# Performance work log

Measured on AMD Instinct MI355X. Metric: run time of the kernel, lower is better.

## Reference

```python
import jax, jax.numpy as jnp
import numpy as np

B, SEQ, NNODES = 4, 12, 1024
SEG_LEN, SEG_NUM = 3, 4
HID, FF, DK, NH, NLAYERS = 64, 2048, 32, 8, 2


def setup_inputs() -> dict:
    key = jax.random.key(0)
    ks = iter(jax.random.split(key, 64))
    def nrm(shape, scale=0.05):
        return jax.random.normal(next(ks), shape, dtype=jnp.float32) * scale
    ones = lambda s: jnp.ones(s, jnp.float32)
    zeros = lambda s: jnp.zeros(s, jnp.float32)
    S, L = 2, NLAYERS
    return {
        'traffic': nrm((B, SEQ, NNODES), 1.0),
        'user': nrm((B, SEQ, NNODES), 1.0),
        'patch_w': nrm((S, HID, SEG_LEN)), 'patch_b': nrm((S, HID)),
        'mha_w': nrm((S, L, 3 * HID, HID)), 'mha_b': nrm((S, L, 3 * HID)),
        'out_w': nrm((S, L, HID, HID)), 'out_b': nrm((S, L, HID)),
        'ff1_w': nrm((S, L, FF, HID)), 'ff1_b': nrm((S, L, FF)),
        'ff2_w': nrm((S, L, HID, FF)), 'ff2_b': nrm((S, L, HID)),
        'ln1_g': ones((S, L, HID)), 'ln1_b': zeros((S, L, HID)),
        'ln2_g': ones((S, L, HID)), 'ln2_b': zeros((S, L, HID)),
        'ga_wq': nrm((S, L, DK, HID)), 'ga_wk': nrm((S, L, DK, HID)), 'ga_wv': nrm((S, L, HID, HID)),
        'ga_ff1_w': nrm((S, L, FF, HID)), 'ga_ff1_b': nrm((S, L, FF)),
        'ga_ff2_w': nrm((S, L, HID, FF)), 'ga_ff2_b': nrm((S, L, HID)),
        'ga_ln1_g': ones((S, L, HID)), 'ga_ln1_b': zeros((S, L, HID)),
        'ga_ln2_g': ones((S, L, HID)), 'ga_ln2_b': zeros((S, L, HID)),
        'ca_wq': nrm((DK, 2 * HID)), 'ca_wk': nrm((DK, 2 * HID)), 'ca_wv': nrm((HID, 2 * HID)),
    }


def _ln(x, g, b, eps=1e-5):
    m = x.mean(-1, keepdims=True)
    v = jnp.mean((x - m) ** 2, -1, keepdims=True)
    return (x - m) / jnp.sqrt(v + eps) * g + b


def _pe(s, d):
    pos = jnp.arange(s, dtype=jnp.float32)[:, None]
    div = jnp.exp(jnp.arange(0, d, 2, dtype=jnp.float32) * (-np.log(10000.0) / d))
    pe = jnp.zeros((s, d), jnp.float32)
    pe = pe.at[:, 0::2].set(jnp.sin(pos * div))
    pe = pe.at[:, 1::2].set(jnp.cos(pos * div))
    return pe


def _mha(x, w, b, wo, bo):
    # standard nn.MultiheadAttention self-attn, batch_first; x: [B,S,H]
    qkv = x @ w.T + b
    q, k, v = jnp.split(qkv, 3, axis=-1)
    def heads(t):
        b_, s_, h_ = t.shape
        return t.reshape(b_, s_, NH, h_ // NH).transpose(0, 2, 1, 3)
    q, k, v = heads(q), heads(k), heads(v)
    scale = 1.0 / jnp.sqrt(jnp.float32(HID // NH))
    att = jax.nn.softmax(jnp.einsum('bhqd,bhkd->bhqk', q, k) * scale, axis=-1)
    o = jnp.einsum('bhqk,bhkd->bhqd', att, v).transpose(0, 2, 1, 3).reshape(x.shape)
    return o @ wo.T + bo


def _enc_layer(x, p):
    # TransformerEncoderLayer_cross, post-norm, dropout=0 (eval)
    x = _ln(x + _mha(x, p['mw'], p['mb'], p['ow'], p['ob']), p['g1'], p['b1'])
    f = jax.nn.relu(x @ p['f1w'].T + p['f1b']) @ p['f2w'].T + p['f2b']
    return _ln(x + f, p['g2'], p['b2'])


def _graph_att(x, p):
    # GraphAttention.forward (bias=None, mask=None, dropout=0)
    q = x @ p['wq'].T
    k = x @ p['wk'].T
    v = x @ p['wv'].T
    dist = jax.nn.softmax(jnp.einsum('bnd,bmd->bnm', q, k) / jnp.sqrt(jnp.float32(DK)), axis=-1)
    att = jnp.einsum('bnm,bmd->bnd', dist, v)
    att = _ln(att, p['g1'], p['b1']) + x
    f = jax.nn.relu(att @ p['f1w'].T + p['f1b']) @ p['f2w'].T + p['f2b']
    return _ln(att + f, p['g2'], p['b2'])


def reference(traffic, user, patch_w, patch_b, mha_w, mha_b, out_w, out_b,
              ff1_w, ff1_b, ff2_w, ff2_b, ln1_g, ln1_b, ln2_g, ln2_b,
              ga_wq, ga_wk, ga_wv, ga_ff1_w, ga_ff1_b, ga_ff2_w, ga_ff2_b,
              ga_ln1_g, ga_ln1_b, ga_ln2_g, ga_ln2_b, ca_wq, ca_wk, ca_wv):
    pe = _pe(SEG_NUM, HID)

    def encode(x, s):
        b, _, d = x.shape
        # DSW_embedding: b (seg_num seg_len) d -> b d seg_num seg_len, then Linear
        seg = x.reshape(b, SEG_NUM, SEG_LEN, d).transpose(0, 3, 1, 2)
        z = seg @ patch_w[s].T + patch_b[s]          # [b, d, seg_num, HID]
        z = z + pe                                    # positional encoding over patches
        for i in range(NLAYERS):
            # temporal attention over the patch axis
            zt = z.reshape(b * d, SEG_NUM, HID)
            zt = _enc_layer(zt, dict(mw=mha_w[s, i], mb=mha_b[s, i], ow=out_w[s, i], ob=out_b[s, i],
                                     f1w=ff1_w[s, i], f1b=ff1_b[s, i], f2w=ff2_w[s, i], f2b=ff2_b[s, i],
                                     g1=ln1_g[s, i], b1=ln1_b[s, i], g2=ln2_g[s, i], b2=ln2_b[s, i]))
            z = zt.reshape(b, d, SEG_NUM, HID)
            # spatial graph attention over the node axis
            zs = z.transpose(0, 2, 1, 3).reshape(b * SEG_NUM, d, HID)
            zs = _graph_att(zs, dict(wq=ga_wq[s, i], wk=ga_wk[s, i], wv=ga_wv[s, i],
                                     f1w=ga_ff1_w[s, i], f1b=ga_ff1_b[s, i], f2w=ga_ff2_w[s, i], f2b=ga_ff2_b[s, i],
                                     g1=ga_ln1_g[s, i], b1=ga_ln1_b[s, i], g2=ga_ln2_g[s, i], b2=ga_ln2_b[s, i]))
            z = zs.reshape(b, SEG_NUM, d, HID).transpose(0, 2, 1, 3)
        return z.mean(axis=2)                         # pool patches -> [b, d, HID]

    enc = jnp.concatenate([encode(traffic, 0), encode(user, 1)], axis=-1)  # [b, d, 2*HID]
    # encoder_attn: SelfAttention(2*HID -> dim_k=32, dim_v=HID)
    q = enc @ ca_wq.T
    k = enc @ ca_wk.T
    v = enc @ ca_wv.T
    dist = jax.nn.softmax(jnp.einsum('bnd,bmd->bnm', q, k) / jnp.sqrt(jnp.float32(DK)), axis=-1)
    return jnp.einsum('bnm,bmd->bnd', dist, v)        # [b, n_nodes, HID]
```

## Files before the change

kernel.cpp:

```cpp
#include <hip/hip_runtime.h>
#include <hip/hip_bf16.h>
#include <math.h>

#define BB 4
#define SEQL 12
#define NN 1024
#define SEGL 3
#define SEGN 4
#define HID 64
#define FFD 2048
#define DKK 32
#define NHH 8
#define HDD 8
#define ZS 1048576

using bf16 = __hip_bfloat16;
__device__ __forceinline__ float b2f(bf16 v) { return __bfloat162float(v); }

typedef __attribute__((ext_vector_type(8))) short s8v;
typedef __attribute__((ext_vector_type(4))) float f4v;
typedef __attribute__((ext_vector_type(4))) unsigned short u4v;

__device__ __forceinline__ unsigned short f2b(float f) {
  bf16 h = __float2bfloat16(f);
  unsigned short u; __builtin_memcpy(&u, &h, 2); return u;
}
__device__ __forceinline__ float us2f(unsigned short u) {
  unsigned int e = ((unsigned int)u) << 16;
  float f; __builtin_memcpy(&f, &e, 4); return f;
}

template <int F>
__device__ __forceinline__ float ldw(const void* p, long i) {
  if (F) return ((const float*)p)[i];
  return b2f(((const bf16*)p)[i]);
}
template <int F>
__device__ __forceinline__ s8v ldfrag(const void* p, long elemOff) {
  if (F) {
    const float* fp = (const float*)p + elemOff;
    f4v u = *(const f4v*)fp, v = *(const f4v*)(fp + 4);
    s8v t;
    t[0]=f2b(u[0]); t[1]=f2b(u[1]); t[2]=f2b(u[2]); t[3]=f2b(u[3]);
    t[4]=f2b(v[0]); t[5]=f2b(v[1]); t[6]=f2b(v[2]); t[7]=f2b(v[3]);
    return t;
  }
  return *(const s8v*)((const unsigned short*)p + elemOff);
}
template <int F>
__device__ __forceinline__ f4v ldb4(const void* p, long i) {
  if (F) return *(const f4v*)((const float*)p + i);
  u4v u = *(const u4v*)((const unsigned short*)p + i);
  f4v r; r[0]=us2f(u[0]); r[1]=us2f(u[1]); r[2]=us2f(u[2]); r[3]=us2f(u[3]);
  return r;
}

__global__ void k_zero(unsigned short* __restrict__ o, int n) {
  int i = blockIdx.x * 256 + threadIdx.x;
  if (i < n) o[i] = 0;
}

__global__ void k_detect(const void* __restrict__ x0, int* __restrict__ flag) {
  int t = threadIdx.x;
  int bad = 0;
  const bf16* p = (const bf16*)x0;
  for (int i = t; i < 512; i += 256) {
    float a = fabsf(b2f(p[i]));
    if (!(a < 1e4f) || (a != 0.f && a < 1e-4f)) bad = 1;
  }
  __shared__ int tot;
  if (t == 0) tot = 0;
  __syncthreads();
  unsigned long long m = __ballot(bad);
  if ((t & 63) == 0) atomicAdd(&tot, __popcll(m));
  __syncthreads();
  if (t == 0) *flag = (tot > 64) ? 1 : 0;
}

template <int F>
__device__ __forceinline__ void wconv_body(const void* __restrict__ w1,
    const void* __restrict__ w2, const void* __restrict__ w3,
    const void* __restrict__ w4, unsigned short* __restrict__ out) {
  int i = blockIdx.x * 256 + threadIdx.x;
  long e8 = (long)i * 8;
  int slot = (int)(e8 >> 17);
  int si = slot >> 2, which = slot & 3;
  long r = e8 & 131071;
  const void* src = (which == 0) ? w1 : (which == 1) ? w2 : (which == 2) ? w3 : w4;
  *(s8v*)(out + e8) = ldfrag<F>(src, (long)si*FFD*HID + r);
}
__global__ __launch_bounds__(256) void k_wconv(const void* w1, const void* w2,
    const void* w3, const void* w4, unsigned short* out,
    const int* __restrict__ flag) {
  if (*flag) wconv_body<1>(w1, w2, w3, w4, out);
  else       wconv_body<0>(w1, w2, w3, w4, out);
}

#define TT 64
#define FRW 64
#define HCS 74

__device__ __forceinline__ void ff_ld(const unsigned short* __restrict__ wc1,
    const unsigned short* __restrict__ wc2, int hb, int srow, int le,
    s8v* r1, s8v* r2) {
  r1[0] = *(const s8v*)(wc1 + (long)(hb + srow)*HID + le*8);
  r1[1] = *(const s8v*)(wc1 + (long)(hb + srow + 8)*HID + le*8);
  r2[0] = *(const s8v*)(wc2 + (long)srow*FFD + hb + le*8);
  r2[1] = *(const s8v*)(wc2 + (long)(srow + 8)*FFD + hb + le*8);
}
__device__ __forceinline__ void ff_wr(char* ldsbuf, int pb, int srow, int swb,
    const s8v* r1, const s8v* r2) {
  char* w1b = ldsbuf + pb*8192;
  char* w2b = ldsbuf + 16384 + pb*8192;
  *(s8v*)(w1b + srow*128 + swb) = r1[0];
  *(s8v*)(w1b + (srow + 8)*128 + swb) = r1[1];
  *(s8v*)(w2b + srow*128 + swb) = r2[0];
  *(s8v*)(w2b + (srow + 8)*128 + swb) = r2[1];
}
template <int F>
__device__ __forceinline__ void ff_compute(const char* ldsbuf, int pb, int hb,
    int col, int quad, int sw, const s8v* bx, unsigned short* hcw,
    const void* __restrict__ B1, long ob1, f4v* acc) {
  const char* w1b = ldsbuf + pb*8192;
  const char* w2b = ldsbuf + 16384 + pb*8192;
#pragma unroll
  for (int t = 0; t < 4; ++t) {
    int row = t*16 + col;
    s8v a10 = *(const s8v*)(w1b + row*128 + ((quad*16) ^ sw));
    s8v a11 = *(const s8v*)(w1b + row*128 + ((64 + quad*16) ^ sw));
    f4v bv = ldb4<F>(B1, ob1 + hb + t*16 + quad*4);
    f4v sv = __builtin_amdgcn_mfma_f32_16x16x32_bf16(a10, bx[0],
               (f4v){0.f,0.f,0.f,0.f}, 0, 0, 0);
    sv = __builtin_amdgcn_mfma_f32_16x16x32_bf16(a11, bx[1], sv, 0, 0, 0);
    unsigned short pk[4];
#pragma unroll
    for (int r = 0; r < 4; ++r) pk[r] = f2b(fmaxf(sv[r] + bv[r], 0.f));
    *(unsigned long long*)&hcw[col*HCS + t*16 + quad*4] =
      (unsigned long long)pk[0] | ((unsigned long long)pk[1] << 16) |
      ((unsigned long long)pk[2] << 32) | ((unsigned long long)pk[3] << 48);
  }
#pragma unroll
  for (int ks2 = 0; ks2 < 2; ++ks2) {
    s8v bh = *(const s8v*)&hcw[col*HCS + ks2*32 + quad*8];
#pragma unroll
    for (int m = 0; m < 4; ++m) {
      int r2 = m*16 + col;
      s8v a2 = *(const s8v*)(w2b + r2*128 + ((ks2*64 + quad*16) ^ sw));
      acc[m] = __builtin_amdgcn_mfma_f32_16x16x32_bf16(a2, bh, acc[m], 0, 0, 0);
    }
  }
}
template <int F>
__device__ __forceinline__ void ff_run(char* ldsbuf,
    const unsigned short* __restrict__ wc1, const unsigned short* __restrict__ wc2,
    const void* __restrict__ B1, long ob1, const s8v* bx, unsigned short* hcw,
    int col, int quad, int sw, int srow, int le, int swb, f4v* acc) {
  s8v c1[2], c2[2], rA1[2], rA2[2], rB1[2], rB2[2];
  ff_ld(wc1, wc2, 0, srow, le, c1, c2);
  ff_wr(ldsbuf, 0, srow, swb, c1, c2);
  ff_ld(wc1, wc2, 64, srow, le, rA1, rA2);
  ff_ld(wc1, wc2, 128, srow, le, rB1, rB2);
  __syncthreads();
  for (int c = 0; c < 32; c += 2) {
    ff_compute<F>(ldsbuf, 0, c*64, col, quad, sw, bx, hcw, B1, ob1, acc);
    ff_wr(ldsbuf, 1, srow, swb, rA1, rA2);
    if (c + 3 < 32) ff_ld(wc1, wc2, (c+3)*64, srow, le, rA1, rA2);
    __syncthreads();
    ff_compute<F>(ldsbuf, 1, (c+1)*64, col, quad, sw, bx, hcw, B1, ob1, acc);
    if (c + 2 < 32) ff_wr(ldsbuf, 0, srow, swb, rB1, rB2);
    if (c + 4 < 32) ff_ld(wc1, wc2, (c+4)*64, srow, le, rB1, rB2);
    __syncthreads();
  }
}

template <int F>
__device__ __forceinline__ void tff_body(float* __restrict__ zb,
    const void* __restrict__ xt, const void* __restrict__ xu,
    const void* __restrict__ pw, const void* __restrict__ pbp,
    const void* __restrict__ W, const void* __restrict__ bq,
    const void* __restrict__ WO, const void* __restrict__ bo,
    const void* __restrict__ g1, const void* __restrict__ b1,
    const unsigned short* __restrict__ wcw, int li,
    const void* __restrict__ B1, const void* __restrict__ B2,
    const void* __restrict__ G, const void* __restrict__ Bt,
    const void* __restrict__ pgf1b, const void* __restrict__ pgf2b,
    const void* __restrict__ pgl2g, const void* __restrict__ pgl2b,
    const void* __restrict__ gwq, const void* __restrict__ gwk,
    const void* __restrict__ gwv,
    unsigned short* __restrict__ qo, unsigned short* __restrict__ ko,
    unsigned short* __restrict__ vto,
    char* lds) {
  int s = blockIdx.x >> 8, blk = blockIdx.x & 255;
  long si = s*2 + li;
  float* z = zb + (long)s*ZS;
  long oW = si*3*HID*HID, obq = si*3*HID, oWO = si*HID*HID, obo = si*HID;
  long og1 = si*HID, ob1 = si*HID;
  const unsigned short* wc1 = wcw + (si*4 + 0)*131072;
  const unsigned short* wc2 = wcw + (si*4 + 1)*131072;
  long fob1 = si*FFD, fob2 = si*HID, fog = si*HID, fobt = si*HID;
  unsigned short (*qkvs)[200] = (unsigned short(*)[200])lds;
  unsigned short (*ao)[72]    = (unsigned short(*)[72])(lds + 25600);
  float (*yb)[68]             = (float(*)[68])(lds + 34816);
  int tid = threadIdx.x;
  int w = tid >> 6, lane = tid & 63;
  int col = lane & 15, quad = lane >> 4;
  long r0 = (long)blk * TT;
  float* stash = (float*)(lds + 59648);
  float* stashW = stash + w*16*68;
  unsigned short* hcw = (unsigned short*)(lds + 32768 + w*2368);
  float* red = (float*)(lds + 42240 + w*4352);
  int lr = lane >> 3, le = lane & 7;
  int srow = w*16 + lr;
  int swb = ((le ^ lr) << 4);
  const int sw = (col & 7) << 4;

  if (li == 0) {
    const void* x = s ? xu : xt;
    long opw = (long)s*HID*SEGL, opb = (long)s*HID;
    float dv = expf((float)(2*(lane >> 1)) * (-logf(10000.f) / (float)HID));
    float pe[4];
#pragma unroll
    for (int g = 0; g < 4; ++g) {
      float ang = (float)g * dv;
      pe[g] = (lane & 1) ? cosf(ang) : sinf(ang);
    }
    float pbv = ldw<F>(pbp, opb + lane);
    float pwv[3];
#pragma unroll
    for (int l = 0; l < 3; ++l) pwv[l] = ldw<F>(pw, opw + lane*3 + l);
#pragma unroll
    for (int rr = 0; rr < 16; ++rr) {
      long tok = r0 + w*16 + rr;
      int b_ = (int)(tok >> 12);
      int n_ = (int)((tok >> 2) & 1023);
      int g_ = (int)(tok & 3);
      float a = pbv;
#pragma unroll
      for (int l = 0; l < 3; ++l)
        a += ldw<F>(x, (long)(b_*SEQL + g_*SEGL + l)*NN + n_) * pwv[l];
      stashW[rr*68 + lane] = a + pe[g_];
    }
    __syncthreads();
  } else {
    long sip = s*2;
    const unsigned short* pw1 = wcw + (sip*4 + 2)*131072;
    const unsigned short* pw2 = wcw + (sip*4 + 3)*131072;
    long pob1 = sip*FFD, pob2 = sip*HID, pog = sip*HID, pobt = sip*HID;
    s8v bxp[2];
    {
      const float* xr = z + (r0 + w*16 + col) * HID;
#pragma unroll
      for (int ks = 0; ks < 2; ++ks) {
        const float* p = xr + ks*32 + quad*8;
        f4v u = *(const f4v*)p, v = *(const f4v*)(p + 4);
        s8v t;
        t[0]=f2b(u[0]); t[1]=f2b(u[1]); t[2]=f2b(u[2]); t[3]=f2b(u[3]);
        t[4]=f2b(v[0]); t[5]=f2b(v[1]); t[6]=f2b(v[2]); t[7]=f2b(v[3]);
        bxp[ks] = t;
      }
    }
    f4v accp[4];
#pragma unroll
    for (int m = 0; m < 4; ++m) accp[m] = (f4v){0.f,0.f,0.f,0.f};
    ff_run<F>(lds, pw1, pw2, pgf1b, pob1, bxp, hcw, col, quad, sw, srow, le, swb, accp);
#pragma unroll
    for (int m = 0; m < 4; ++m)
      *(f4v*)&red[col*68 + m*16 + quad*4] = accp[m];
    float pgg = ldw<F>(pgl2g, pog + lane), pbb = ldw<F>(pgl2b, pobt + lane);
    float pb2 = ldw<F>(pgf2b, pob2 + lane);
#pragma unroll
    for (int rr = 0; rr < 16; ++rr) {
      long grow = r0 + w*16 + rr;
      float val = red[rr*68 + lane] + pb2 + z[grow*HID + lane];
      float sm = val;
#pragma unroll
      for (int off = 32; off; off >>= 1) sm += __shfl_xor(sm, off);
      float m = sm * (1.f/HID);
      float d = val - m;
      float sq = d*d;
#pragma unroll
      for (int off = 32; off; off >>= 1) sq += __shfl_xor(sq, off);
      float rv = rsqrtf(sq*(1.f/HID) + 1e-5f);
      stashW[rr*68 + lane] = d*rv*pgg + pbb;
    }
    __syncthreads();
  }

  s8v bx[4][2];
#pragma unroll
  for (int mt = 0; mt < 4; ++mt) {
    const float* xr = &stash[(mt*16 + col)*68];
#pragma unroll
    for (int ks = 0; ks < 2; ++ks) {
      const float* p = xr + ks*32 + quad*8;
      f4v u = *(const f4v*)p, v = *(const f4v*)(p + 4);
      s8v t;
      t[0]=f2b(u[0]); t[1]=f2b(u[1]); t[2]=f2b(u[2]); t[3]=f2b(u[3]);
      t[4]=f2b(v[0]); t[5]=f2b(v[1]); t[6]=f2b(v[2]); t[7]=f2b(v[3]);
      bx[mt][ks] = t;
    }
  }
#pragma unroll
  for (int nt = 0; nt < 3; ++nt) {
    int cbase = (w*3 + nt) * 16;
    s8v aw[2];
#pragma unroll
    for (int ks = 0; ks < 2; ++ks)
      aw[ks] = ldfrag<F>(W, oW + (long)(cbase + col)*HID + ks*32 + quad*8);
    f4v bv = ldb4<F>(bq, obq + cbase + quad*4);
#pragma unroll
    for (int mt = 0; mt < 4; ++mt) {
      f4v sv = (f4v){0.f,0.f,0.f,0.f};
#pragma unroll
      for (int ks = 0; ks < 2; ++ks)
        sv = __builtin_amdgcn_mfma_f32_16x16x32_bf16(aw[ks], bx[mt][ks], sv, 0, 0, 0);
      unsigned short pk[4];
#pragma unroll
      for (int r = 0; r < 4; ++r) pk[r] = f2b(sv[r] + bv[r]);
      *(unsigned long long*)&qkvs[mt*16 + col][cbase + quad*4] =
        (unsigned long long)pk[0] | ((unsigned long long)pk[1] << 16) |
        ((unsigned long long)pk[2] << 32) | ((unsigned long long)pk[3] << 48);
    }
  }
  __syncthreads();
  if (tid < 128) {
    int gi = tid >> 3, hd = tid & 7;
    int tl = gi * 4;
    float qv[4][8], kv[4][8], vv[4][8];
#pragma unroll
    for (int t4 = 0; t4 < 4; ++t4) {
      s8v qq = *(const s8v*)&qkvs[tl + t4][hd*8];
      s8v kk = *(const s8v*)&qkvs[tl + t4][64 + hd*8];
      s8v vq = *(const s8v*)&qkvs[tl + t4][128 + hd*8];
#pragma unroll
      for (int e = 0; e < 8; ++e) {
        qv[t4][e] = us2f((unsigned short)qq[e]);
        kv[t4][e] = us2f((unsigned short)kk[e]);
        vv[t4][e] = us2f((unsigned short)vq[e]);
      }
    }
    const float sc8 = 0.3535533905932738f;
#pragma unroll
    for (int qt = 0; qt < 4; ++qt) {
      float sc[4]; float mx = -1e30f;
#pragma unroll
      for (int kt = 0; kt < 4; ++kt) {
        float d = 0;
#pragma unroll
        for (int e = 0; e < 8; ++e) d += qv[qt][e]*kv[kt][e];
        sc[kt] = d*sc8; mx = fmaxf(mx, sc[kt]);
      }
      float se = 0;
#pragma unroll
      for (int kt = 0; kt < 4; ++kt) { sc[kt] = expf(sc[kt]-mx); se += sc[kt]; }
      float inv = 1.f/se;
      s8v outp;
#pragma unroll
      for (int e = 0; e < 8; ++e) {
        float o = 0;
#pragma unroll
        for (int kt = 0; kt < 4; ++kt) o += sc[kt]*vv[kt][e];
        outp[e] = (short)f2b(o*inv);
      }
      *(s8v*)&ao[tl + qt][hd*8] = outp;
    }
  }
  __syncthreads();
  s8v awo[2];
#pragma unroll
  for (int ks = 0; ks < 2; ++ks)
    awo[ks] = ldfrag<F>(WO, oWO + (long)(w*16 + col)*HID + ks*32 + quad*8);
  f4v bov = ldb4<F>(bo, obo + w*16 + quad*4);
#pragma unroll
  for (int mt = 0; mt < 4; ++mt) {
    f4v ov = (f4v){0.f,0.f,0.f,0.f};
#pragma unroll
    for (int ks = 0; ks < 2; ++ks) {
      s8v bao = *(const s8v*)&ao[mt*16 + col][ks*32 + quad*8];
      ov = __builtin_amdgcn_mfma_f32_16x16x32_bf16(awo[ks], bao, ov, 0, 0, 0);
    }
    f4v yv;
#pragma unroll
    for (int r = 0; r < 4; ++r) yv[r] = ov[r] + bov[r];
    *(f4v*)&yb[mt*16 + col][w*16 + quad*4] = yv;
  }
  __syncthreads();
  {
    float gg = ldw<F>(g1, og1 + lane), bb2 = ldw<F>(b1, ob1 + lane);
#pragma unroll
    for (int rr = 0; rr < 16; ++rr) {
      int row = w*16 + rr;
      float val = yb[row][lane] + stashW[rr*68 + lane];
      float sm = val;
#pragma unroll
      for (int off = 32; off; off >>= 1) sm += __shfl_xor(sm, off);
      float m = sm*(1.f/HID);
      float d = val - m, sq = d*d;
#pragma unroll
      for (int off = 32; off; off >>= 1) sq += __shfl_xor(sq, off);
      float rv = rsqrtf(sq*(1.f/HID) + 1e-5f);
      stashW[rr*68 + lane] = d*rv*gg + bb2;
    }
  }
  __syncthreads();

  s8v bx2[2];
#pragma unroll
  for (int ks = 0; ks < 2; ++ks) {
    const float* p = &stashW[col*68 + ks*32 + quad*8];
    f4v u = *(const f4v*)p, v = *(const f4v*)(p + 4);
    s8v t;
    t[0]=f2b(u[0]); t[1]=f2b(u[1]); t[2]=f2b(u[2]); t[3]=f2b(u[3]);
    t[4]=f2b(v[0]); t[5]=f2b(v[1]); t[6]=f2b(v[2]); t[7]=f2b(v[3]);
    bx2[ks] = t;
  }

  f4v acc[4];
#pragma unroll
  for (int m = 0; m < 4; ++m) acc[m] = (f4v){0.f,0.f,0.f,0.f};
  ff_run<F>(lds, wc1, wc2, B1, fob1, bx2, hcw, col, quad, sw, srow, le, swb, acc);

#pragma unroll
  for (int m = 0; m < 4; ++m)
    *(f4v*)&red[col*68 + m*16 + quad*4] = acc[m];
  float* finb = (float*)lds;
  {
    float fgg = ldw<F>(G, fog + lane), fbbt = ldw<F>(Bt, fobt + lane);
    float b2v = ldw<F>(B2, fob2 + lane);
#pragma unroll
    for (int rr = 0; rr < 16; ++rr) {
      long grow = r0 + w*16 + rr;
      float val = red[rr*68 + lane] + b2v + stashW[rr*68 + lane];
      float sm = val;
#pragma unroll
      for (int off = 32; off; off >>= 1) sm += __shfl_xor(sm, off);
      float m = sm * (1.f/HID);
      float d = val - m;
      float sq = d*d;
#pragma unroll
      for (int off = 32; off; off >>= 1) sq += __shfl_xor(sq, off);
      float rv = rsqrtf(sq*(1.f/HID) + 1e-5f);
      float fin = d*rv*fgg + fbbt;
      z[grow*HID + lane] = fin;
      finb[(w*16 + rr)*68 + lane] = fin;
    }
  }
  __syncthreads();

  long oq = si*DKK*HID, okk = si*DKK*HID, ovv = si*HID*HID;
  s8v bx3[4][2];
#pragma unroll
  for (int rt = 0; rt < 4; ++rt)
#pragma unroll
    for (int ks = 0; ks < 2; ++ks) {
      const float* p = &finb[(rt*16 + col)*68 + ks*32 + quad*8];
      f4v u = *(const f4v*)p, v = *(const f4v*)(p + 4);
      s8v t;
      t[0]=f2b(u[0]); t[1]=f2b(u[1]); t[2]=f2b(u[2]); t[3]=f2b(u[3]);
      t[4]=f2b(v[0]); t[5]=f2b(v[1]); t[6]=f2b(v[2]); t[7]=f2b(v[3]);
      bx3[rt][ks] = t;
    }
#pragma unroll
  for (int tt = 0; tt < 2; ++tt) {
    int ct = w*2 + tt;
    const void* wp; long wo; int co; int kind;
    if (ct < 2)      { wp = gwq; wo = oq;  co = ct*16;      kind = 0; }
    else if (ct < 4) { wp = gwk; wo = okk; co = (ct-2)*16;  kind = 1; }
    else             { wp = gwv; wo = ovv; co = (ct-4)*16;  kind = 2; }
    s8v aw[2];
#pragma unroll
    for (int ks = 0; ks < 2; ++ks)
      aw[ks] = ldfrag<F>(wp, wo + (long)(co + col)*HID + ks*32 + quad*8);
#pragma unroll
    for (int rt = 0; rt < 4; ++rt) {
      f4v sv = (f4v){0.f,0.f,0.f,0.f};
#pragma unroll
      for (int ks = 0; ks < 2; ++ks)
        sv = __builtin_amdgcn_mfma_f32_16x16x32_bf16(aw[ks], bx3[rt][ks], sv, 0, 0, 0);
      long tok2 = r0 + rt*16 + col;
      int b_ = (int)(tok2 >> 12);
      int n_ = (int)((tok2 >> 2) & 1023);
      int g_ = (int)(tok2 & 3);
      int sgl = s*16 + b_*4 + g_;
      if (kind == 2) {
        long vbase = (long)sgl*HID*NN;
#pragma unroll
        for (int r = 0; r < 4; ++r)
          vto[vbase + (long)(co + quad*4 + r)*NN + n_] = f2b(sv[r]);
      } else {
        long row = (long)sgl*NN + n_;
        unsigned short pk[4];
#pragma unroll
        for (int r = 0; r < 4; ++r) pk[r] = f2b(sv[r]);
        unsigned short* dst = kind ? ko : qo;
        *(unsigned long long*)&dst[row*DKK + co + quad*4] =
          (unsigned long long)pk[0] | ((unsigned long long)pk[1] << 16) |
          ((unsigned long long)pk[2] << 32) | ((unsigned long long)pk[3] << 48);
      }
    }
  }
}
__global__ __launch_bounds__(256) void k_tff(float* __restrict__ z,
    const void* xt, const void* xu, const void* pw, const void* pbp,
    const void* W, const void* bqkv, const void* WO, const void* bo,
    const void* g1, const void* b1,
    const unsigned short* __restrict__ wcw, int li,
    const void* B1, const void* B2, const void* G, const void* Bt,
    const void* pgf1b, const void* pgf2b, const void* pgl2g, const void* pgl2b,
    const void* gwq, const void* gwk, const void* gwv,
    unsigned short* qo, unsigned short* ko, unsigned short* vto,
    const int* __restrict__ flag) {
  __shared__ __attribute__((aligned(16))) char lds[77056];
  if (*flag) tff_body<1>(z, xt, xu, pw, pbp, W, bqkv, WO, bo, g1, b1, wcw, li,
                         B1, B2, G, Bt, pgf1b, pgf2b, pgl2g, pgl2b,
                         gwq, gwk, gwv, qo, ko, vto, lds);
  else       tff_body<0>(z, xt, xu, pw, pbp, W, bqkv, WO, bo, g1, b1, wcw, li,
                         B1, B2, G, Bt, pgf1b, pgf2b, pgl2g, pgl2b,
                         gwq, gwk, gwv, qo, ko, vto, lds);
}

template <int F>
__device__ __forceinline__ void ffmfma_body(float* __restrict__ xb,
    const unsigned short* __restrict__ wcw, int li, int wsel,
    const void* __restrict__ B1, const void* __restrict__ B2,
    const void* __restrict__ G, const void* __restrict__ Bt,
    float* __restrict__ enc, int dop,
    char* ldsbuf) {
  int s = blockIdx.x >> 8, blk = blockIdx.x & 255;
  long si = s*2 + li;
  float* x = xb + (long)s*ZS;
  const unsigned short* wc1 = wcw + (si*4 + wsel)*131072;
  const unsigned short* wc2 = wcw + (si*4 + wsel + 1)*131072;
  long ob1 = si*FFD, ob2 = si*HID, og = si*HID, obt = si*HID;
  int tid = threadIdx.x;
  int w = tid >> 6, lane = tid & 63;
  int col = lane & 15, quad = lane >> 4;
  long r0 = (long)blk * FRW;
  unsigned short* hcw = (unsigned short*)(ldsbuf + 32768 + w*2368);
  float* red = (float*)(ldsbuf + w*4352);

  long tokc = r0 + w*16 + col;
  s8v bx[2];
  {
    const float* xr = x + tokc * HID;
#pragma unroll
    for (int ks = 0; ks < 2; ++ks) {
      const float* p = xr + ks*32 + quad*8;
      f4v u = *(const f4v*)p, v = *(const f4v*)(p + 4);
      s8v t;
      t[0]=f2b(u[0]); t[1]=f2b(u[1]); t[2]=f2b(u[2]); t[3]=f2b(u[3]);
      t[4]=f2b(v[0]); t[5]=f2b(v[1]); t[6]=f2b(v[2]); t[7]=f2b(v[3]);
      bx[ks] = t;
    }
  }

  int lr = lane >> 3;
  int le = lane & 7;
  int srow = w*16 + lr;
  int swb = ((le ^ lr) << 4);
  const int sw = (col & 7) << 4;

  f4v acc[4];
#pragma unroll
  for (int m = 0; m < 4; ++m) acc[m] = (f4v){0.f,0.f,0.f,0.f};
  ff_run<F>(ldsbuf, wc1, wc2, B1, ob1, bx, hcw, col, quad, sw, srow, le, swb, acc);

#pragma unroll
  for (int m = 0; m < 4; ++m)
    *(f4v*)&red[col*68 + m*16 + quad*4] = acc[m];
  float gg = ldw<F>(G, og + lane), bbt = ldw<F>(Bt, obt + lane);
  float b2v = ldw<F>(B2, ob2 + lane);
  float pacc[4] = {0.f,0.f,0.f,0.f};
#pragma unroll
  for (int rr = 0; rr < 16; ++rr) {
    long grow = r0 + w*16 + rr;
    float val = red[rr*68 + lane] + b2v + x[grow*HID + lane];
    float sm = val;
#pragma unroll
    for (int off = 32; off; off >>= 1) sm += __shfl_xor(sm, off);
    float m = sm * (1.f/HID);
    float d = val - m;
    float sq = d*d;
#pragma unroll
    for (int off = 32; off; off >>= 1) sq += __shfl_xor(sq, off);
    float rv = rsqrtf(sq*(1.f/HID) + 1e-5f);
    float fin = d*rv*gg + bbt;
    x[grow*HID + lane] = fin;
    pacc[rr >> 2] += fin;
  }
  if (dop) {
#pragma unroll
    for (int j = 0; j < 4; ++j) {
      long tok = r0 + w*16 + j*4;
      enc[(tok >> 2)*(2*HID) + s*HID + lane] = pacc[j]*0.25f;
    }
  }
}
__global__ __launch_bounds__(256) void k_ffmfma(float* __restrict__ x,
    const unsigned short* __restrict__ wcw, int li, int wsel,
    const void* B1, const void* B2, const void* G, const void* Bt,
    float* enc, int dop, const int* __restrict__ flag) {
  __shared__ __attribute__((aligned(16))) char ldsbuf[42240];
  if (*flag) ffmfma_body<1>(x, wcw, li, wsel, B1, B2, G, Bt, enc, dop, ldsbuf);
  else       ffmfma_body<0>(x, wcw, li, wsel, B1, B2, G, Bt, enc, dop, ldsbuf);
}

__global__ __launch_bounds__(512) void k_gattn(float* __restrict__ zb,
    const unsigned short* __restrict__ qb, const unsigned short* __restrict__ kb,
    const unsigned short* __restrict__ vtb,
    const void* __restrict__ g1, const void* __restrict__ b1, int li,
    const int* __restrict__ flag) {
  int f = *flag;
  __shared__ unsigned short pl[2][8][16][74];
  __shared__ float accb[8][16][66];
  __shared__ float lb[8][16];
  int tid = threadIdx.x;
  int w = tid >> 6, lane = tid & 63;
  int col = lane & 15, quad = lane >> 4;
  int qt = w >> 2, kh = w & 3;
  int sg = blockIdx.x >> 5;
  int s = sg >> 4, bg = sg & 15;
  int n0 = (blockIdx.x & 31) * 32;
  long si = s*2 + li;
  float* z = zb + (long)s*ZS;
  long og1 = si*HID, ob1 = si*HID;
  long gbase = (long)sg * NN;
  const unsigned short* vrow = vtb + (long)sg*HID*NN;

  s8v aq = *(const s8v*)(qb + (gbase + n0 + qt*16 + col)*DKK + quad*8);

  f4v acc[4];
#pragma unroll
  for (int t = 0; t < 4; ++t) acc[t] = (f4v){0.f,0.f,0.f,0.f};
  float psum[4] = {0.f,0.f,0.f,0.f};
  const float rs = 0.17677669529663687f;
  const int cbeg = kh * 256;

#pragma unroll 2
  for (int it = 0; it < 4; ++it) {
    int c0 = cbeg + it*64;
    int pb = it & 1;
    f4v s4[4];
#pragma unroll
    for (int nt = 0; nt < 4; ++nt) {
      s8v bk = *(const s8v*)(kb + (gbase + c0 + nt*16 + col)*DKK + quad*8);
      s4[nt] = __builtin_amdgcn_mfma_f32_16x16x32_bf16(aq, bk,
                (f4v){0.f,0.f,0.f,0.f}, 0, 0, 0);
    }
#pragma unroll
    for (int r = 0; r < 4; ++r) {
      float p0 = expf(s4[0][r]*rs), p1 = expf(s4[1][r]*rs);
      float p2 = expf(s4[2][r]*rs), p3 = expf(s4[3][r]*rs);
      psum[r] += (p0 + p1) + (p2 + p3);
      int row = quad*4 + r;
      pl[pb][w][row][col]      = f2b(p0);
      pl[pb][w][row][16 + col] = f2b(p1);
      pl[pb][w][row][32 + col] = f2b(p2);
      pl[pb][w][row][48 + col] = f2b(p3);
    }
#pragma unroll
    for (int ks = 0; ks < 2; ++ks) {
      s8v ap = *(const s8v*)&pl[pb][w][col][ks*32 + quad*8];
#pragma unroll
      for (int nt = 0; nt < 4; ++nt) {
        s8v bv = *(const s8v*)(vrow + (long)(nt*16 + col)*NN + c0 + ks*32 + quad*8);
        acc[nt] = __builtin_amdgcn_mfma_f32_16x16x32_bf16(ap, bv, acc[nt], 0, 0, 0);
      }
    }
  }

#pragma unroll
  for (int r = 0; r < 4; ++r) {
    float v = psum[r];
#pragma unroll
    for (int off = 1; off < 16; off <<= 1) v += __shfl_xor(v, off);
    psum[r] = v;
  }
#pragma unroll
  for (int t = 0; t < 4; ++t)
#pragma unroll
    for (int r = 0; r < 4; ++r)
      accb[w][quad*4 + r][t*16 + col] = acc[t][r];
  if (col == 0) {
#pragma unroll
    for (int r = 0; r < 4; ++r) lb[w][quad*4 + r] = psum[r];
  }
  __syncthreads();

  int b = bg >> 2, g = bg & 3;
  float gg = f ? ((const float*)g1)[og1 + lane] : b2f(((const bf16*)g1)[og1 + lane]);
  float bb = f ? ((const float*)b1)[ob1 + lane] : b2f(((const bf16*)b1)[ob1 + lane]);
#pragma unroll
  for (int rr = 0; rr < 4; ++rr) {
    int rl = w*4 + rr;
    int qtt = rl >> 4, lrr = rl & 15;
    float a = accb[4*qtt][lrr][lane] + accb[4*qtt + 1][lrr][lane]
            + accb[4*qtt + 2][lrr][lane] + accb[4*qtt + 3][lrr][lane];
    float l = lb[4*qtt][lrr] + lb[4*qtt + 1][lrr]
            + lb[4*qtt + 2][lrr] + lb[4*qtt + 3][lrr];
    float val = a / l;
    float s2 = val;
#pragma unroll
    for (int off = 32; off; off >>= 1) s2 += __shfl_xor(s2, off);
    float m = s2*(1.f/HID);
    float d = val - m, sq = d*d;
#pragma unroll
    for (int off = 32; off; off >>= 1) sq += __shfl_xor(sq, off);
    float r = rsqrtf(sq*(1.f/HID) + 1e-5f);
    float* zp = z + ((long)(b*NN + n0 + rl)*SEGN + g)*HID;
    zp[lane] = d*r*gg + bb + zp[lane];
  }
}

template <int F>
__device__ __forceinline__ void fqkv_body(const float* __restrict__ enc,
    const void* __restrict__ wq, const void* __restrict__ wk,
    const void* __restrict__ wv,
    unsigned short* __restrict__ q, unsigned short* __restrict__ k,
    unsigned short* __restrict__ vt, float* xs) {
  long r = blockIdx.x;
  int t = threadIdx.x;
  xs[t] = enc[r*128 + t];
  __syncthreads();
  if (t < 32) {
    long wr = (long)t*128; float a = 0;
    for (int e = 0; e < 128; ++e) a += xs[e]*ldw<F>(wq, wr + e);
    q[r*DKK + t] = f2b(a);
  } else if (t < 64) {
    long wr = (long)(t-32)*128; float a = 0;
    for (int e = 0; e < 128; ++e) a += xs[e]*ldw<F>(wk, wr + e);
    k[r*DKK + (t-32)] = f2b(a);
  } else {
    long wr = (long)(t-64)*128; float a = 0;
    for (int e = 0; e < 128; ++e) a += xs[e]*ldw<F>(wv, wr + e);
    vt[((r >> 10)*HID + (t-64))*NN + (r & 1023)] = f2b(a);
  }
}
__global__ __launch_bounds__(128) void k_fqkv(const float* __restrict__ enc,
    const void* wq, const void* wk, const void* wv,
    unsigned short* q, unsigned short* k, unsigned short* vt,
    const int* __restrict__ flag) {
  __shared__ float xs[2*HID];
  if (*flag) fqkv_body<1>(enc, wq, wk, wv, q, k, vt, xs);
  else       fqkv_body<0>(enc, wq, wk, wv, q, k, vt, xs);
}

__global__ __launch_bounds__(512) void k_fattn(
    const unsigned short* __restrict__ qb, const unsigned short* __restrict__ kb,
    const unsigned short* __restrict__ vtb, void* __restrict__ outp,
    const int* __restrict__ flag) {
  __shared__ unsigned short pl[2][8][16][74];
  __shared__ float accb[8][16][66];
  __shared__ float lb[8][16];
  int tid = threadIdx.x;
  int w = tid >> 6, lane = tid & 63;
  int col = lane & 15, quad = lane >> 4;
  int qt = w >> 2, kh = w & 3;
  int b = blockIdx.x >> 5;
  int n0 = (blockIdx.x & 31) * 32;
  long gbase = (long)b * NN;
  const unsigned short* vrow = vtb + (long)b*HID*NN;

  s8v aq = *(const s8v*)(qb + (gbase + n0 + qt*16 + col)*DKK + quad*8);

  f4v acc[4];
#pragma unroll
  for (int t = 0; t < 4; ++t) acc[t] = (f4v){0.f,0.f,0.f,0.f};
  float psum[4] = {0.f,0.f,0.f,0.f};
  const float rs = 0.17677669529663687f;
  const int cbeg = kh * 256;

#pragma unroll 2
  for (int it = 0; it < 4; ++it) {
    int c0 = cbeg + it*64;
    int pb = it & 1;
    f4v s4[4];
#pragma unroll
    for (int nt = 0; nt < 4; ++nt) {
      s8v bk = *(const s8v*)(kb + (gbase + c0 + nt*16 + col)*DKK + quad*8);
      s4[nt] = __builtin_amdgcn_mfma_f32_16x16x32_bf16(aq, bk,
                (f4v){0.f,0.f,0.f,0.f}, 0, 0, 0);
    }
#pragma unroll
    for (int r = 0; r < 4; ++r) {
      float p0 = expf(s4[0][r]*rs), p1 = expf(s4[1][r]*rs);
      float p2 = expf(s4[2][r]*rs), p3 = expf(s4[3][r]*rs);
      psum[r] += (p0 + p1) + (p2 + p3);
      int row = quad*4 + r;
      pl[pb][w][row][col]      = f2b(p0);
      pl[pb][w][row][16 + col] = f2b(p1);
      pl[pb][w][row][32 + col] = f2b(p2);
      pl[pb][w][row][48 + col] = f2b(p3);
    }
#pragma unroll
    for (int ks = 0; ks < 2; ++ks) {
      s8v ap = *(const s8v*)&pl[pb][w][col][ks*32 + quad*8];
#pragma unroll
      for (int nt = 0; nt < 4; ++nt) {
        s8v bv = *(const s8v*)(vrow + (long)(nt*16 + col)*NN + c0 + ks*32 + quad*8);
        acc[nt] = __builtin_amdgcn_mfma_f32_16x16x32_bf16(ap, bv, acc[nt], 0, 0, 0);
      }
    }
  }

#pragma unroll
  for (int r = 0; r < 4; ++r) {
    float v = psum[r];
#pragma unroll
    for (int off = 1; off < 16; off <<= 1) v += __shfl_xor(v, off);
    psum[r] = v;
  }
#pragma unroll
  for (int t = 0; t < 4; ++t)
#pragma unroll
    for (int r = 0; r < 4; ++r)
      accb[w][quad*4 + r][t*16 + col] = acc[t][r];
  if (col == 0) {
#pragma unroll
    for (int r = 0; r < 4; ++r) lb[w][quad*4 + r] = psum[r];
  }
  __syncthreads();

  int f = *flag;
#pragma unroll
  for (int rr = 0; rr < 4; ++rr) {
    int rl = w*4 + rr;
    int qtt = rl >> 4, lrr = rl & 15;
    float a = accb[4*qtt][lrr][lane] + accb[4*qtt + 1][lrr][lane]
            + accb[4*qtt + 2][lrr][lane] + accb[4*qtt + 3][lrr][lane];
    float l = lb[4*qtt][lrr] + lb[4*qtt + 1][lrr]
            + lb[4*qtt + 2][lrr] + lb[4*qtt + 3][lrr];
    float val = a / l;
    long idx = (gbase + n0 + rl)*HID + lane;
    if (f) ((float*)outp)[idx] = val;
    else   ((bf16*)outp)[idx] = __float2bfloat16(val);
  }
}

extern "C" void kernel_launch(void* const* d_in, const int* in_sizes, int n_in,
                              void* d_out, int out_size, void* d_ws, size_t ws_size,
                              hipStream_t stream) {
  static const int EXP[30] = {
    49152, 49152, 384, 128, 49152, 768, 16384, 256,
    524288, 8192, 524288, 256, 256, 256, 256, 256,
    8192, 8192, 16384, 524288, 8192, 524288, 256, 256,
    256, 256, 256, 4096, 4096, 8192
  };
  const size_t NEED = (size_t)(2*ZS + 524288 + 524288 + 524288 + 1048576 + 1048576) * 4 + 64;
  bool ok = (n_in == 30) && (ws_size >= NEED) && (out_size == BB*NN*HID);
  if (ok) for (int i = 0; i < 30; ++i) ok = ok && (in_sizes[i] == EXP[i]);
  if (!ok) {
    k_zero<<<(BB*NN*HID + 255)/256, 256, 0, stream>>>((unsigned short*)d_out, BB*NN*HID);
    return;
  }

  float* z   = (float*)d_ws;
  float* enc = z   + 2*ZS;
  float* qb  = enc + 524288;
  float* kb  = qb  + 524288;
  float* vb  = kb  + 524288;
  float* wcf = vb  + 1048576;
  int*  flag = (int*)(wcf + 1048576);
  unsigned short* wcw = (unsigned short*)wcf;

  k_detect<<<1, 256, 0, stream>>>(d_in[0], flag);

  const void *i_traffic=d_in[0], *i_user=d_in[1], *i_pw=d_in[2], *i_pb=d_in[3],
    *i_mw=d_in[4], *i_mb=d_in[5], *i_ow=d_in[6], *i_ob=d_in[7], *i_f1w=d_in[8],
    *i_f1b=d_in[9], *i_f2w=d_in[10], *i_f2b=d_in[11], *i_l1g=d_in[12],
    *i_l1b=d_in[13], *i_l2g=d_in[14], *i_l2b=d_in[15], *i_gwq=d_in[16],
    *i_gwk=d_in[17], *i_gwv=d_in[18], *i_gf1w=d_in[19], *i_gf1b=d_in[20],
    *i_gf2w=d_in[21], *i_gf2b=d_in[22], *i_gl1g=d_in[23], *i_gl1b=d_in[24],
    *i_gl2g=d_in[25], *i_gl2b=d_in[26], *i_cwq=d_in[27], *i_cwk=d_in[28],
    *i_cwv=d_in[29];

  k_wconv<<<1024, 256, 0, stream>>>(i_f1w, i_f2w, i_gf1w, i_gf2w, wcw, flag);

  k_tff<<<512, 256, 0, stream>>>(z,
      i_traffic, i_user, i_pw, i_pb,
      i_mw, i_mb, i_ow, i_ob,
      i_l1g, i_l1b, wcw, 0, i_f1b, i_f2b, i_l2g, i_l2b,
      i_gf1b, i_gf2b, i_gl2g, i_gl2b,
      i_gwq, i_gwk, i_gwv,
      (unsigned short*)qb, (unsigned short*)kb, (unsigned short*)vb, flag);
  k_gattn<<<1024, 512, 0, stream>>>(z,
      (const unsigned short*)qb, (const unsigned short*)kb,
      (const unsigned short*)vb, i_gl1g, i_gl1b, 0, flag);
  k_tff<<<512, 256, 0, stream>>>(z,
      i_traffic, i_user, i_pw, i_pb,
      i_mw, i_mb, i_ow, i_ob,
      i_l1g, i_l1b, wcw, 1, i_f1b, i_f2b, i_l2g, i_l2b,
      i_gf1b, i_gf2b, i_gl2g, i_gl2b,
      i_gwq, i_gwk, i_gwv,
      (unsigned short*)qb, (unsigned short*)kb, (unsigned short*)vb, flag);
  k_gattn<<<1024, 512, 0, stream>>>(z,
      (const unsigned short*)qb, (const unsigned short*)kb,
      (const unsigned short*)vb, i_gl1g, i_gl1b, 1, flag);
  k_ffmfma<<<512, 256, 0, stream>>>(z, wcw, 1, 2,
      i_gf1b, i_gf2b, i_gl2g, i_gl2b, enc, 1, flag);

  k_fqkv<<<BB*NN, 128, 0, stream>>>(enc, i_cwq, i_cwk, i_cwv,
      (unsigned short*)qb, (unsigned short*)kb, (unsigned short*)vb, flag);
  k_fattn<<<BB*32, 512, 0, stream>>>((const unsigned short*)qb,
      (const unsigned short*)kb, (unsigned short*)vb, d_out, flag);
}
```

Before: 566.8 us.

## Fuse final-layer graph attention with graph feed-forward and pooling kernel

Replaces the last k_gattn launch and the following k_ffmfma launch with a single k_gaf kernel. Each block computes softmax attention over all nodes for its 16-token tile, applies the residual layer norm, stashes the result in LDS, then runs the feed-forward MFMA and the second layer norm before writing the pooled encoder output directly. This drops one launch and the round trip of z through global memory. In exchange it uses fewer, larger-LDS blocks (512×256 instead of 1024×512 for attention), which may lower occupancy and parallelism in the attention phase.

```diff
diff --git a/kernel.cpp b/kernel.cpp
--- a/kernel.cpp
+++ b/kernel.cpp
@@ -520,61 +520,143 @@
 }
 
 template <int F>
-__device__ __forceinline__ void ffmfma_body(float* __restrict__ xb,
-    const unsigned short* __restrict__ wcw, int li, int wsel,
+__device__ __forceinline__ void gaf_body(float* __restrict__ zb,
+    const unsigned short* __restrict__ qb, const unsigned short* __restrict__ kb,
+    const unsigned short* __restrict__ vtb,
+    const void* __restrict__ g1, const void* __restrict__ b1,
+    const unsigned short* __restrict__ wcw,
     const void* __restrict__ B1, const void* __restrict__ B2,
     const void* __restrict__ G, const void* __restrict__ Bt,
-    float* __restrict__ enc, int dop,
-    char* ldsbuf) {
+    float* __restrict__ enc, char* lds) {
   int s = blockIdx.x >> 8, blk = blockIdx.x & 255;
-  long si = s*2 + li;
-  float* x = xb + (long)s*ZS;
-  const unsigned short* wc1 = wcw + (si*4 + wsel)*131072;
-  const unsigned short* wc2 = wcw + (si*4 + wsel + 1)*131072;
-  long ob1 = si*FFD, ob2 = si*HID, og = si*HID, obt = si*HID;
+  long si = s*2 + 1;
+  float* z = zb + (long)s*ZS;
+  long r0 = (long)blk * TT;
+  int b_ = blk >> 6;
+  int n0 = (blk & 63) * 16;
   int tid = threadIdx.x;
   int w = tid >> 6, lane = tid & 63;
   int col = lane & 15, quad = lane >> 4;
-  long r0 = (long)blk * FRW;
-  unsigned short* hcw = (unsigned short*)(ldsbuf + 32768 + w*2368);
-  float* red = (float*)(ldsbuf + w*4352);
-
-  long tokc = r0 + w*16 + col;
-  s8v bx[2];
+  unsigned short (*plw)[16][74] = (unsigned short(*)[16][74])(lds + w*4736);
+  float* obw = (float*)(lds + 18944 + w*4352);
+  float* lbw = (float*)(lds + 36352 + w*64);
+  float* stash = (float*)(lds + 42240);
+  float* stashW = stash + w*16*68;
+  unsigned short* hcw = (unsigned short*)(lds + 32768 + w*2368);
+  float* red = (float*)(lds + w*4352);
+  long og1 = si*HID, obn1 = si*HID;
+
+  long sgw = (long)(s*16 + b_*4 + w);
+  long gbaseW = sgw * NN;
+  const unsigned short* vrow = vtb + sgw*(long)HID*NN;
+  s8v aq = *(const s8v*)(qb + (gbaseW + n0 + col)*DKK + quad*8);
+  f4v acc[4];
+#pragma unroll
+  for (int t = 0; t < 4; ++t) acc[t] = (f4v){0.f,0.f,0.f,0.f};
+  float psum[4] = {0.f,0.f,0.f,0.f};
+  const float rs = 0.17677669529663687f;
+
+#pragma unroll 2
+  for (int it = 0; it < 16; ++it) {
+    int c0 = it*64;
+    int pb = it & 1;
+    f4v s4[4];
+#pragma unroll
+    for (int nt = 0; nt < 4; ++nt) {
+      s8v bk = *(const s8v*)(kb + (gbaseW + c0 + nt*16 + col)*DKK + quad*8);
+      s4[nt] = __builtin_amdgcn_mfma_f32_16x16x32_bf16(aq, bk,
+                (f4v){0.f,0.f,0.f,0.f}, 0, 0, 0);
+    }
+#pragma unroll
+    for (int r = 0; r < 4; ++r) {
+      float p0 = expf(s4[0][r]*rs), p1 = expf(s4[1][r]*rs);
+      float p2 = expf(s4[2][r]*rs), p3 = expf(s4[3][r]*rs);
+      psum[r] += (p0 + p1) + (p2 + p3);
+      int row = quad*4 + r;
+      plw[pb][row][col]      = f2b(p0);
+      plw[pb][row][16 + col] = f2b(p1);
+      plw[pb][row][32 + col] = f2b(p2);
+      plw[pb][row][48 + col] = f2b(p3);
+    }
+#pragma unroll
+    for (int ks = 0; ks < 2; ++ks) {
+      s8v ap = *(const s8v*)&plw[pb][col][ks*32 + quad*8];
+#pragma unroll
+      for (int nt = 0; nt < 4; ++nt) {
+        s8v bv = *(const s8v*)(vrow + (long)(nt*16 + col)*NN + c0 + ks*32 + quad*8);
+        acc[nt] = __builtin_amdgcn_mfma_f32_16x16x32_bf16(ap, bv, acc[nt], 0, 0, 0);
+      }
+    }
+  }
+
+#pragma unroll
+  for (int r = 0; r < 4; ++r) {
+    float v = psum[r];
+#pragma unroll
+    for (int off = 1; off < 16; off <<= 1) v += __shfl_xor(v, off);
+    psum[r] = v;
+  }
+  if (col == 0) {
+#pragma unroll
+    for (int r = 0; r < 4; ++r) lbw[quad*4 + r] = psum[r];
+  }
+#pragma unroll
+  for (int t = 0; t < 4; ++t)
+#pragma unroll
+    for (int r = 0; r < 4; ++r)
+      obw[(quad*4 + r)*68 + t*16 + col] = acc[t][r];
   {
-    const float* xr = x + tokc * HID;
-#pragma unroll
-    for (int ks = 0; ks < 2; ++ks) {
-      const float* p = xr + ks*32 + quad*8;
-      f4v u = *(const f4v*)p, v = *(const f4v*)(p + 4);
-      s8v t;
-      t[0]=f2b(u[0]); t[1]=f2b(u[1]); t[2]=f2b(u[2]); t[3]=f2b(u[3]);
-      t[4]=f2b(v[0]); t[5]=f2b(v[1]); t[6]=f2b(v[2]); t[7]=f2b(v[3]);
-      bx[ks] = t;
-    }
-  }
-
-  int lr = lane >> 3;
-  int le = lane & 7;
+    float gg = ldw<F>(g1, og1 + lane), bb = ldw<F>(b1, obn1 + lane);
+#pragma unroll
+    for (int rr = 0; rr < 16; ++rr) {
+      float val = obw[rr*68 + lane] / lbw[rr];
+      float sm = val;
+#pragma unroll
+      for (int off = 32; off; off >>= 1) sm += __shfl_xor(sm, off);
+      float m = sm*(1.f/HID);
+      float d = val - m, sq = d*d;
+#pragma unroll
+      for (int off = 32; off; off >>= 1) sq += __shfl_xor(sq, off);
+      float rv = rsqrtf(sq*(1.f/HID) + 1e-5f);
+      long tok = r0 + rr*4 + w;
+      stash[(rr*4 + w)*68 + lane] = d*rv*gg + bb + z[tok*HID + lane];
+    }
+  }
+  __syncthreads();
+
+  const unsigned short* wc1 = wcw + (si*4 + 2)*131072;
+  const unsigned short* wc2 = wcw + (si*4 + 3)*131072;
+  long fob1 = si*FFD, fob2 = si*HID, fog = si*HID, fobt = si*HID;
+  int lr = lane >> 3, le = lane & 7;
   int srow = w*16 + lr;
   int swb = ((le ^ lr) << 4);
   const int sw = (col & 7) << 4;
 
-  f4v acc[4];
-#pragma unroll
-  for (int m = 0; m < 4; ++m) acc[m] = (f4v){0.f,0.f,0.f,0.f};
-  ff_run<F>(ldsbuf, wc1, wc2, B1, ob1, bx, hcw, col, quad, sw, srow, le, swb, acc);
+  s8v bx2[2];
+#pragma unroll
+  for (int ks = 0; ks < 2; ++ks) {
+    const float* p = &stashW[col*68 + ks*32 + quad*8];
+    f4v u = *(const f4v*)p, v = *(const f4v*)(p + 4);
+    s8v t;
+    t[0]=f2b(u[0]); t[1]=f2b(u[1]); t[2]=f2b(u[2]); t[3]=f2b(u[3]);
+    t[4]=f2b(v[0]); t[5]=f2b(v[1]); t[6]=f2b(v[2]); t[7]=f2b(v[3]);
+    bx2[ks] = t;
+  }
+
+  f4v acf[4];
+#pragma unroll
+  for (int m = 0; m < 4; ++m) acf[m] = (f4v){0.f,0.f,0.f,0.f};
+  ff_run<F>(lds, wc1, wc2, B1, fob1, bx2, hcw, col, quad, sw, srow, le, swb, acf);
 
 #pragma unroll
   for (int m = 0; m < 4; ++m)
-    *(f4v*)&red[col*68 + m*16 + quad*4] = acc[m];
-  float gg = ldw<F>(G, og + lane), bbt = ldw<F>(Bt, obt + lane);
-  float b2v = ldw<F>(B2, ob2 + lane);
+    *(f4v*)&red[col*68 + m*16 + quad*4] = acf[m];
+  float gg2 = ldw<F>(G, fog + lane), bbt2 = ldw<F>(Bt, fobt + lane);
+  float b2v = ldw<F>(B2, fob2 + lane);
   float pacc[4] = {0.f,0.f,0.f,0.f};
 #pragma unroll
   for (int rr = 0; rr < 16; ++rr) {
-    long grow = r0 + w*16 + rr;
-    float val = red[rr*68 + lane] + b2v + x[grow*HID + lane];
+    float val = red[rr*68 + lane] + b2v + stashW[rr*68 + lane];
     float sm = val;
 #pragma unroll
     for (int off = 32; off; off >>= 1) sm += __shfl_xor(sm, off);
@@ -584,25 +666,24 @@
 #pragma unroll
     for (int off = 32; off; off >>= 1) sq += __shfl_xor(sq, off);
     float rv = rsqrtf(sq*(1.f/HID) + 1e-5f);
-    float fin = d*rv*gg + bbt;
-    x[grow*HID + lane] = fin;
-    pacc[rr >> 2] += fin;
-  }
-  if (dop) {
-#pragma unroll
-    for (int j = 0; j < 4; ++j) {
-      long tok = r0 + w*16 + j*4;
-      enc[(tok >> 2)*(2*HID) + s*HID + lane] = pacc[j]*0.25f;
-    }
-  }
-}
-__global__ __launch_bounds__(256) void k_ffmfma(float* __restrict__ x,
-    const unsigned short* __restrict__ wcw, int li, int wsel,
+    pacc[rr >> 2] += d*rv*gg2 + bbt2;
+  }
+#pragma unroll
+  for (int j = 0; j < 4; ++j) {
+    long tok = r0 + w*16 + j*4;
+    enc[(tok >> 2)*(2*HID) + s*HID + lane] = pacc[j]*0.25f;
+  }
+}
+__global__ __launch_bounds__(256) void k_gaf(float* __restrict__ z,
+    const unsigned short* __restrict__ qb, const unsigned short* __restrict__ kb,
+    const unsigned short* __restrict__ vtb,
+    const void* g1, const void* b1,
+    const unsigned short* __restrict__ wcw,
     const void* B1, const void* B2, const void* G, const void* Bt,
-    float* enc, int dop, const int* __restrict__ flag) {
-  __shared__ __attribute__((aligned(16))) char ldsbuf[42240];
-  if (*flag) ffmfma_body<1>(x, wcw, li, wsel, B1, B2, G, Bt, enc, dop, ldsbuf);
-  else       ffmfma_body<0>(x, wcw, li, wsel, B1, B2, G, Bt, enc, dop, ldsbuf);
+    float* enc, const int* __restrict__ flag) {
+  __shared__ __attribute__((aligned(16))) char lds[59648];
+  if (*flag) gaf_body<1>(z, qb, kb, vtb, g1, b1, wcw, B1, B2, G, Bt, enc, lds);
+  else       gaf_body<0>(z, qb, kb, vtb, g1, b1, wcw, B1, B2, G, Bt, enc, lds);
 }
 
 __global__ __launch_bounds__(512) void k_gattn(float* __restrict__ zb,
@@ -893,11 +974,10 @@
       i_gf1b, i_gf2b, i_gl2g, i_gl2b,
       i_gwq, i_gwk, i_gwv,
       (unsigned short*)qb, (unsigned short*)kb, (unsigned short*)vb, flag);
-  k_gattn<<<1024, 512, 0, stream>>>(z,
+  k_gaf<<<512, 256, 0, stream>>>(z,
       (const unsigned short*)qb, (const unsigned short*)kb,
-      (const unsigned short*)vb, i_gl1g, i_gl1b, 1, flag);
-  k_ffmfma<<<512, 256, 0, stream>>>(z, wcw, 1, 2,
-      i_gf1b, i_gf2b, i_gl2g, i_gl2b, enc, 1, flag);
+      (const unsigned short*)vb, i_gl1g, i_gl1b, wcw,
+      i_gf1b, i_gf2b, i_gl2g, i_gl2b, enc, flag);
 
   k_fqkv<<<BB*NN, 128, 0, stream>>>(enc, i_cwq, i_cwk, i_cwv,
       (unsigned short*)qb, (unsigned short*)kb, (unsigned short*)vb, flag);
```

Measured after the change: 587.3 us. 1.04x slower.
